# Kernel tuning notes

Measured on AMD Instinct MI355X. Metric: run time of the kernel, lower is better.

The kernel has to match this reference:

```python
import jax, jax.numpy as jnp
import numpy as np

H, D_MODEL, LEN_Q, LEN_K, D_K, D_V = 16, 1024, 512, 2048, 64, 64
B = 4

def setup_inputs() -> dict:
    key = jax.random.key(0)
    ks = jax.random.split(key, 16)
    s = 0.02
    return {
        "Q": jax.random.normal(ks[0], (B, LEN_Q, D_MODEL), jnp.float32),
        "K": jax.random.normal(ks[1], (B, LEN_K, D_MODEL), jnp.float32),
        "V": jax.random.normal(ks[2], (B, LEN_K, D_MODEL), jnp.float32),
        "node_num": LEN_Q,
        "mask": jax.random.randint(ks[3], (B, LEN_K), 0, 2, jnp.int32),
        # params (stored as [in, out] so y = x @ W + b)
        "Wq": jax.random.normal(ks[4], (D_MODEL, H * D_K), jnp.float32) * s,
        "bq": jnp.zeros((H * D_K,), jnp.float32),
        "Wk": jax.random.normal(ks[5], (D_MODEL, H * D_K), jnp.float32) * s,
        "bk": jnp.zeros((H * D_K,), jnp.float32),
        "Wv": jax.random.normal(ks[6], (D_MODEL, H * D_V), jnp.float32) * s,
        "bv": jnp.zeros((H * D_V,), jnp.float32),
        "Wo": jax.random.normal(ks[7], (H * D_V, D_MODEL), jnp.float32) * s,
        "bo": jnp.zeros((D_MODEL,), jnp.float32),
        "gamma": jnp.ones((D_MODEL,), jnp.float32),
        "beta": jnp.zeros((D_MODEL,), jnp.float32),
    }

def _layernorm(x, gamma, beta, eps=1e-5):
    mu = jnp.mean(x, axis=-1, keepdims=True)
    var = jnp.mean((x - mu) ** 2, axis=-1, keepdims=True)
    return (x - mu) * jax.lax.rsqrt(var + eps) * gamma + beta

def reference(Q, K, V, node_num, mask, Wq, bq, Wk, bk, Wv, bv, Wo, bo, gamma, beta):
    b, lq, _ = Q.shape
    lk = K.shape[1]
    q = (Q @ Wq + bq).reshape(b, lq, H, D_K)   # [B, Lq, h, dk]
    k = (K @ Wk + bk).reshape(b, lk, H, D_K)   # [B, Lk, h, dk]
    v = (V @ Wv + bv).reshape(b, lk, H, D_V)   # [B, Lk, h, dv]
    scores = jnp.einsum('bqhd,bkhd->bhqk', q, k) / jnp.sqrt(jnp.float32(D_K))
    scores = jnp.where(mask[:, None, None, :] == 0, -jnp.inf, scores)
    alpha = jax.nn.softmax(scores, axis=-1)    # [B, h, Lq, Lk]
    out = jnp.einsum('bhqk,bkhd->bqhd', alpha, v).reshape(b, lq, H * D_V)
    out = out @ Wo + bo + Q                    # dropout is identity (eval)
    return _layernorm(out, gamma, beta)
```

## Files before the change

### kernel.cpp

```cpp
#include <hip/hip_runtime.h>

typedef __attribute__((ext_vector_type(8))) __bf16 bf16x8;
typedef __attribute__((ext_vector_type(4))) float f32x4;
typedef __attribute__((ext_vector_type(8))) unsigned short u16x8;

__device__ __forceinline__ float bf2f(unsigned short h) {
  union { unsigned int u; float f; } a; a.u = ((unsigned int)h) << 16; return a.f;
}
__device__ __forceinline__ unsigned short f2bf(float f) {
  __bf16 h = (__bf16)f;
  unsigned short u; __builtin_memcpy(&u, &h, 2); return u;
}
__device__ __forceinline__ float fast_exp2(float x) {
#if __has_builtin(__builtin_amdgcn_exp2f)
  return __builtin_amdgcn_exp2f(x);
#else
  return exp2f(x);
#endif
}
__device__ __forceinline__ bf16x8 ld_frag(const unsigned short* p) {
  bf16x8 r; __builtin_memcpy(&r, p, 16); return r;
}
__device__ __forceinline__ void cp16(unsigned short* dst, const unsigned short* src) {
  u16x8 t; __builtin_memcpy(&t, src, 16); __builtin_memcpy(dst, &t, 16);
}

#if __has_builtin(__builtin_amdgcn_global_load_lds)
typedef __attribute__((address_space(3))) unsigned int lds_u32;
typedef const __attribute__((address_space(1))) unsigned int glb_u32;
__device__ __forceinline__ void gload16(const unsigned short* g, unsigned short* l) {
  __builtin_amdgcn_global_load_lds((glb_u32*)g, (lds_u32*)l, 16, 0, 0);
}
#else
__device__ __forceinline__ void gload16(const unsigned short* g, unsigned short* l) {
  cp16(l, g);
}
#endif

__global__ __launch_bounds__(256) void prep_kernel(
    const float* __restrict__ Q, const float* __restrict__ K, const float* __restrict__ V,
    const float* __restrict__ w0, const float* __restrict__ w1,
    const float* __restrict__ w2, const float* __restrict__ w3,
    unsigned short* __restrict__ qb, unsigned short* __restrict__ kb,
    unsigned short* __restrict__ vb, unsigned short* __restrict__ wt)
{
  __shared__ unsigned short tile[64 * 65];
  const int bid = blockIdx.x;
  const int t = threadIdx.x;
  if (bid < 9216) {
    const float* in; unsigned short* out; int i;
    if (bid < 1024)      { in = Q; out = qb; i = bid * 256 + t; }
    else if (bid < 5120) { in = K; out = kb; i = (bid - 1024) * 256 + t; }
    else                 { in = V; out = vb; i = (bid - 5120) * 256 + t; }
    float tf[8]; __builtin_memcpy(tf, &in[(size_t)i * 8], 32);
    unsigned short tu[8];
#pragma unroll
    for (int j = 0; j < 8; j++) tu[j] = f2bf(tf[j]);
    __builtin_memcpy(&out[(size_t)i * 8], tu, 16);
    return;
  }
  const int t4 = bid - 9216;
  const int z = t4 >> 8;
  const float* in = (z == 0) ? w0 : (z == 1) ? w1 : (z == 2) ? w2 : w3;
  unsigned short* o = wt + (size_t)z * 1048576;
  const int dim = 1024;
  const int n0 = (t4 & 15) * 64, k0 = ((t4 >> 4) & 15) * 64;
#pragma unroll
  for (int e = 0; e < 16; e++) {
    int idx = e * 256 + t;
    int i = idx >> 6, j = idx & 63;
    tile[i * 65 + j] = f2bf(in[(size_t)(k0 + i) * dim + n0 + j]);
  }
  __syncthreads();
#pragma unroll
  for (int e = 0; e < 16; e++) {
    int idx = e * 256 + t;
    int i = idx >> 6, j = idx & 63;
    o[(size_t)(n0 + i) * dim + k0 + j] = tile[j * 65 + i];
  }
}

__global__ __launch_bounds__(256, 4) void projqk_kernel(
    const unsigned short* __restrict__ qb,
    const unsigned short* __restrict__ kb,
    const unsigned short* __restrict__ WT4,
    const float* __restrict__ bq, const float* __restrict__ bk,
    unsigned short* __restrict__ qp,
    unsigned short* __restrict__ ktiles)
{
  __shared__ unsigned short pool[12288];
  const int bid = blockIdx.x;
  const int tid  = threadIdx.x;
  const int wave = tid >> 6;
  const int lane = tid & 63;
  const int quad = lane >> 4;
  const int l16  = lane & 15;
  const int K = 1024;
  const f32x4 fz = {0.0f, 0.0f, 0.0f, 0.0f};
  const int srow0 = tid >> 2;
  const int scol  = (tid & 3) * 8;

  if (bid < 512) {
    const int m0 = (bid & 31) * 64;
    const int n0 = (bid >> 5) * 64;
    const int wm = (wave & 1) * 32;
    const int wn = (wave >> 1) * 32;
    f32x4 acc[2][2];
#pragma unroll
    for (int i = 0; i < 2; i++)
#pragma unroll
      for (int j = 0; j < 2; j++) acc[i][j] = fz;

    auto stage = [&](int bf, int k0) {
      unsigned short* Asb = pool + bf * 2048;
      unsigned short* Bsb = pool + 4096 + bf * 2048;
      gload16(&qb[(size_t)(m0 + srow0) * K + k0 + scol], &Asb[srow0 * 32 + scol]);
      gload16(&WT4[(size_t)(n0 + srow0) * K + k0 + scol], &Bsb[srow0 * 32 + scol]);
    };
    const int NT = K >> 5;
    stage(0, 0);
    for (int kt = 0; kt < NT; ++kt) {
      const int cur = kt & 1;
      if (kt + 1 < NT) {
        stage(cur ^ 1, (kt + 1) << 5);
        asm volatile("s_waitcnt vmcnt(2)" ::: "memory");
      } else {
        asm volatile("s_waitcnt vmcnt(0)" ::: "memory");
      }
      __builtin_amdgcn_s_barrier();
      const unsigned short* Asb = pool + cur * 2048;
      const unsigned short* Bsb = pool + 4096 + cur * 2048;
      bf16x8 afr[2], bfr[2];
#pragma unroll
      for (int mt = 0; mt < 2; mt++) afr[mt] = ld_frag(&Asb[(wm + mt * 16 + l16) * 32 + quad * 8]);
#pragma unroll
      for (int nt = 0; nt < 2; nt++) bfr[nt] = ld_frag(&Bsb[(wn + nt * 16 + l16) * 32 + quad * 8]);
#pragma unroll
      for (int mt = 0; mt < 2; mt++)
#pragma unroll
        for (int nt = 0; nt < 2; nt++)
          acc[mt][nt] = __builtin_amdgcn_mfma_f32_16x16x32_bf16(afr[mt], bfr[nt], acc[mt][nt], 0, 0, 0);
      __builtin_amdgcn_s_barrier();
    }
    const float cscale = 0.18033688011112042f;
#pragma unroll
    for (int nt = 0; nt < 2; nt++) {
      int col = n0 + wn + nt * 16 + l16;
      float bv = bq[col];
#pragma unroll
      for (int mt = 0; mt < 2; mt++) {
        int rowb = m0 + wm + mt * 16 + quad * 4;
#pragma unroll
        for (int r = 0; r < 4; r++)
          qp[(size_t)(rowb + r) * 1024 + col] = f2bf((acc[mt][nt][r] + bv) * cscale);
      }
    }
  } else {
    const int tb = bid - 512;
    const int m0 = (tb & 63) * 128;
    const int n0 = (tb >> 6) * 64;
    const int wm = (wave & 1) * 64;
    const int wn = (wave >> 1) * 32;
    const unsigned short* BT = WT4 + 1048576;
    f32x4 acc[4][2];
#pragma unroll
    for (int i = 0; i < 4; i++)
#pragma unroll
      for (int j = 0; j < 2; j++) acc[i][j] = fz;

    const int srow1 = srow0 + 64;
    auto stage = [&](int bf, int k0) {
      unsigned short* Asb = pool + bf * 4096;
      unsigned short* Bsb = pool + 8192 + bf * 2048;
      gload16(&kb[(size_t)(m0 + srow0) * K + k0 + scol], &Asb[srow0 * 32 + scol]);
      gload16(&kb[(size_t)(m0 + srow1) * K + k0 + scol], &Asb[srow1 * 32 + scol]);
      gload16(&BT[(size_t)(n0 + srow0) * K + k0 + scol], &Bsb[srow0 * 32 + scol]);
    };
    const int NT = K >> 5;
    stage(0, 0);
    for (int kt = 0; kt < NT; ++kt) {
      const int cur = kt & 1;
      if (kt + 1 < NT) {
        stage(cur ^ 1, (kt + 1) << 5);
        asm volatile("s_waitcnt vmcnt(3)" ::: "memory");
      } else {
        asm volatile("s_waitcnt vmcnt(0)" ::: "memory");
      }
      __builtin_amdgcn_s_barrier();
      const unsigned short* Asb = pool + cur * 4096;
      const unsigned short* Bsb = pool + 8192 + cur * 2048;
      bf16x8 afr[4], bfr[2];
#pragma unroll
      for (int mt = 0; mt < 4; mt++) afr[mt] = ld_frag(&Asb[(wm + mt * 16 + l16) * 32 + quad * 8]);
#pragma unroll
      for (int nt = 0; nt < 2; nt++) bfr[nt] = ld_frag(&Bsb[(wn + nt * 16 + l16) * 32 + quad * 8]);
#pragma unroll
      for (int mt = 0; mt < 4; mt++)
#pragma unroll
        for (int nt = 0; nt < 2; nt++)
          acc[mt][nt] = __builtin_amdgcn_mfma_f32_16x16x32_bf16(afr[mt], bfr[nt], acc[mt][nt], 0, 0, 0);
      __builtin_amdgcn_s_barrier();
    }
#pragma unroll
    for (int nt = 0; nt < 2; nt++) {
      const int col = n0 + wn + nt * 16 + l16;
      const float bvv = bk[col];
      const int h  = col >> 6;
      const int dk = col & 63;
      const int kc = dk >> 5;
      const int dq = (dk >> 3) & 3;
      const int de = dk & 7;
#pragma unroll
      for (int mt = 0; mt < 4; mt++) {
#pragma unroll
        for (int r = 0; r < 4; r++) {
          const int row = m0 + wm + mt * 16 + quad * 4 + r;
          const int bb = row >> 11, key = row & 2047;
          const size_t tile = ((size_t)((bb * 16 + h) * 32 + (key >> 6))) * 4096;
          const int knt = (key & 63) >> 4;
          const int kl16 = key & 15;
          ktiles[tile + ((size_t)((knt * 2 + kc) * 64 + dq * 16 + kl16)) * 8 + de] =
              f2bf(acc[mt][nt][r] + bvv);
        }
      }
    }
  }
}

__global__ __launch_bounds__(256) void gemm_bt64_kernel(
    const unsigned short* __restrict__ A,
    const unsigned short* __restrict__ BT,
    const float* __restrict__ bias,
    unsigned short* __restrict__ C,
    int M, int N, int K, float cscale)
{
  __shared__ unsigned short As[2][64 * 32];
  __shared__ unsigned short Bs[2][64 * 32];
  const int tid  = threadIdx.x;
  const int wave = tid >> 6;
  const int lane = tid & 63;
  const int quad = lane >> 4;
  const int l16  = lane & 15;
  const int m0 = blockIdx.x * 64;
  const int n0 = blockIdx.y * 64;
  const int wm = (wave & 1) * 32;
  const int wn = (wave >> 1) * 32;

  const f32x4 fz = {0.0f, 0.0f, 0.0f, 0.0f};
  f32x4 acc[2][2];
#pragma unroll
  for (int i = 0; i < 2; i++)
#pragma unroll
    for (int j = 0; j < 2; j++) acc[i][j] = fz;

  const int srow0 = tid >> 2;
  const int scol  = (tid & 3) * 8;

  auto stage = [&](int bf, int k0) {
    gload16(&A[(size_t)(m0 + srow0) * K + k0 + scol], &As[bf][srow0 * 32 + scol]);
    gload16(&BT[(size_t)(n0 + srow0) * K + k0 + scol], &Bs[bf][srow0 * 32 + scol]);
  };

  const int NT = K >> 5;
  stage(0, 0);
  for (int kt = 0; kt < NT; ++kt) {
    const int cur = kt & 1;
    if (kt + 1 < NT) {
      stage(cur ^ 1, (kt + 1) << 5);
      asm volatile("s_waitcnt vmcnt(2)" ::: "memory");
    } else {
      asm volatile("s_waitcnt vmcnt(0)" ::: "memory");
    }
    __builtin_amdgcn_s_barrier();
    bf16x8 afr[2], bfr[2];
#pragma unroll
    for (int mt = 0; mt < 2; mt++) afr[mt] = ld_frag(&As[cur][(wm + mt * 16 + l16) * 32 + quad * 8]);
#pragma unroll
    for (int nt = 0; nt < 2; nt++) bfr[nt] = ld_frag(&Bs[cur][(wn + nt * 16 + l16) * 32 + quad * 8]);
#pragma unroll
    for (int mt = 0; mt < 2; mt++)
#pragma unroll
      for (int nt = 0; nt < 2; nt++)
        acc[mt][nt] = __builtin_amdgcn_mfma_f32_16x16x32_bf16(afr[mt], bfr[nt], acc[mt][nt], 0, 0, 0);
    __builtin_amdgcn_s_barrier();
  }

#pragma unroll
  for (int nt = 0; nt < 2; nt++) {
    int col = n0 + wn + nt * 16 + l16;
    float bv = bias[col];
#pragma unroll
    for (int mt = 0; mt < 2; mt++) {
      int rowb = m0 + wm + mt * 16 + quad * 4;
#pragma unroll
      for (int r = 0; r < 4; r++)
        C[(size_t)(rowb + r) * N + col] = f2bf((acc[mt][nt][r] + bv) * cscale);
    }
  }
}

__global__ __launch_bounds__(256, 4) void gemm_vt_kernel(
    const unsigned short* __restrict__ A,
    const unsigned short* __restrict__ BT,
    const float* __restrict__ bias,
    unsigned short* __restrict__ vt)
{
  __shared__ unsigned short pool[12288];
  const int K = 1024;
  const int tid  = threadIdx.x;
  const int wave = tid >> 6;
  const int lane = tid & 63;
  const int quad = lane >> 4;
  const int l16  = lane & 15;
  const int m0 = blockIdx.x * 128;
  const int n0 = blockIdx.y * 64;
  const int wm = (wave & 1) * 64;
  const int wn = (wave >> 1) * 32;

  const f32x4 fz = {0.0f, 0.0f, 0.0f, 0.0f};
  f32x4 acc[4][2];
#pragma unroll
  for (int i = 0; i < 4; i++)
#pragma unroll
    for (int j = 0; j < 2; j++) acc[i][j] = fz;

  const int srow0 = tid >> 2;
  const int srow1 = srow0 + 64;
  const int scol  = (tid & 3) * 8;

  auto stage = [&](int bf, int k0) {
    unsigned short* Asb = pool + bf * 6144;
    unsigned short* Bsb = Asb + 4096;
    gload16(&A[(size_t)(m0 + srow0) * K + k0 + scol], &Asb[srow0 * 32 + scol]);
    gload16(&A[(size_t)(m0 + srow1) * K + k0 + scol], &Asb[srow1 * 32 + scol]);
    gload16(&BT[(size_t)(n0 + srow0) * K + k0 + scol], &Bsb[srow0 * 32 + scol]);
  };

  const int NT = K >> 5;
  stage(0, 0);
  for (int kt = 0; kt < NT; ++kt) {
    const int cur = kt & 1;
    if (kt + 1 < NT) {
      stage(cur ^ 1, (kt + 1) << 5);
      asm volatile("s_waitcnt vmcnt(3)" ::: "memory");
    } else {
      asm volatile("s_waitcnt vmcnt(0)" ::: "memory");
    }
    __builtin_amdgcn_s_barrier();
    const unsigned short* Asb = pool + cur * 6144;
    const unsigned short* Bsb = Asb + 4096;
    bf16x8 afr[4], bfr[2];
#pragma unroll
    for (int mt = 0; mt < 4; mt++) afr[mt] = ld_frag(&Asb[(wm + mt * 16 + l16) * 32 + quad * 8]);
#pragma unroll
    for (int nt = 0; nt < 2; nt++) bfr[nt] = ld_frag(&Bsb[(wn + nt * 16 + l16) * 32 + quad * 8]);
#pragma unroll
    for (int mt = 0; mt < 4; mt++)
#pragma unroll
      for (int nt = 0; nt < 2; nt++)
        acc[mt][nt] = __builtin_amdgcn_mfma_f32_16x16x32_bf16(afr[mt], bfr[nt], acc[mt][nt], 0, 0, 0);
    __builtin_amdgcn_s_barrier();
  }

  unsigned short* Ts = pool + wave * 2304;
#pragma unroll
  for (int nt = 0; nt < 2; nt++) {
    const float bvv = bias[n0 + wn + nt * 16 + l16];
#pragma unroll
    for (int mt = 0; mt < 4; mt++)
#pragma unroll
      for (int r = 0; r < 4; r++)
        Ts[(nt * 16 + l16) * 72 + mt * 16 + quad * 4 + r] = f2bf(acc[mt][nt][r] + bvv);
  }
  {
    const int R0 = m0 + wm;
    const int b  = R0 >> 11;
    const int ktile = (R0 & 2047) >> 6;
    const int h = n0 >> 6;
    const int dv_local = lane >> 1;
    const int kc = lane & 1;
    const int dv = wn + dv_local;
    const int dvt = dv >> 4, vl16 = dv & 15;
    const size_t vtile = ((size_t)((b * 16 + h) * 32 + ktile)) * 4096;
#pragma unroll
    for (int jb = 0; jb < 4; jb++) {
      const size_t dst = vtile + ((size_t)((dvt * 2 + kc) * 64 + jb * 16 + vl16)) * 8;
      cp16((unsigned short*)&vt[dst], &Ts[dv_local * 72 + kc * 32 + jb * 8]);
    }
  }
}

__global__ __launch_bounds__(512) void attn_kernel(
    const unsigned short* __restrict__ qp,
    const unsigned short* __restrict__ kp,
    const unsigned short* __restrict__ vt,
    const int* __restrict__ mask,
    unsigned short* __restrict__ attn)
{
  __shared__ unsigned short Kb[2][4096];
  __shared__ unsigned short Vb[2][4096];
  __shared__ int Ms[2048];
  __shared__ unsigned short Ps[8][16 * 72];

  const int tid  = threadIdx.x;
  const int wave = tid >> 6;
  const int lane = tid & 63;
  const int quad = lane >> 4;
  const int l16  = lane & 15;
  const int bid  = blockIdx.x;
  const int bh = bid & 63;
  const int qg = bid >> 6;
  const int b = bh >> 4, h = bh & 15;

  bf16x8 aq[2];
  {
    const size_t qbase = ((size_t)(b * 512 + qg * 128 + wave * 16 + l16)) * 1024 + h * 64;
#pragma unroll
    for (int kc = 0; kc < 2; kc++)
      aq[kc] = ld_frag(&qp[qbase + kc * 32 + quad * 8]);
  }
  {
    const unsigned short* mg = (const unsigned short*)(mask + b * 2048);
    unsigned short* ml = (unsigned short*)Ms;
    gload16(mg + tid * 8, ml + tid * 8);
  }
  asm volatile("s_waitcnt vmcnt(0)" ::: "memory");

  const size_t kvbase = (size_t)bh * 131072;
  auto stageKV = [&](int bf, int kt) {
    const unsigned short* ksrc = kp + kvbase + (size_t)kt * 4096;
    const unsigned short* vsrc = vt + kvbase + (size_t)kt * 4096;
    gload16(ksrc + tid * 8, &Kb[bf][tid * 8]);
    gload16(vsrc + tid * 8, &Vb[bf][tid * 8]);
  };

  const f32x4 fz = {0.0f, 0.0f, 0.0f, 0.0f};
  float l_i[4];
  f32x4 O[4];
#pragma unroll
  for (int r = 0; r < 4; r++) { l_i[r] = 0.0f; O[r] = fz; }

  stageKV(0, 0);
  for (int kt = 0; kt < 32; ++kt) {
    const int cur = kt & 1;
    if (kt + 1 < 32) {
      stageKV(cur ^ 1, kt + 1);
      asm volatile("s_waitcnt vmcnt(2)" ::: "memory");
    } else {
      asm volatile("s_waitcnt vmcnt(0)" ::: "memory");
    }
    __builtin_amdgcn_s_barrier();

    int mk[4];
#pragma unroll
    for (int nt = 0; nt < 4; nt++) mk[nt] = Ms[kt * 64 + nt * 16 + l16];

    f32x4 s[4];
#pragma unroll
    for (int nt = 0; nt < 4; nt++) s[nt] = fz;
    __builtin_amdgcn_s_setprio(1);
#pragma unroll
    for (int nt = 0; nt < 4; nt++)
#pragma unroll
      for (int kc = 0; kc < 2; kc++) {
        bf16x8 bk = ld_frag(&Kb[cur][(nt * 2 + kc) * 512 + lane * 8]);
        s[nt] = __builtin_amdgcn_mfma_f32_16x16x32_bf16(aq[kc], bk, s[nt], 0, 0, 0);
      }
    __builtin_amdgcn_s_setprio(0);

#pragma unroll
    for (int nt = 0; nt < 4; nt++) {
      bool ok = (mk[nt] != 0);
#pragma unroll
      for (int r = 0; r < 4; r++) {
        float p = ok ? fast_exp2(s[nt][r]) : 0.0f;
        l_i[r] += p;
        Ps[wave][(quad * 4 + r) * 72 + nt * 16 + l16] = f2bf(p);
      }
    }

    bf16x8 ap[2];
#pragma unroll
    for (int kc = 0; kc < 2; kc++)
      ap[kc] = ld_frag(&Ps[wave][l16 * 72 + kc * 32 + quad * 8]);
    __builtin_amdgcn_s_setprio(1);
#pragma unroll
    for (int dvt = 0; dvt < 4; dvt++)
#pragma unroll
      for (int kc = 0; kc < 2; kc++) {
        bf16x8 bvf = ld_frag(&Vb[cur][(dvt * 2 + kc) * 512 + lane * 8]);
        O[dvt] = __builtin_amdgcn_mfma_f32_16x16x32_bf16(ap[kc], bvf, O[dvt], 0, 0, 0);
      }
    __builtin_amdgcn_s_setprio(0);
    __builtin_amdgcn_s_barrier();
  }

#pragma unroll
  for (int off = 1; off < 16; off <<= 1)
#pragma unroll
    for (int r = 0; r < 4; r++) l_i[r] += __shfl_xor(l_i[r], off);

  const int growb = b * 512 + qg * 128 + wave * 16 + quad * 4;
#pragma unroll
  for (int r = 0; r < 4; r++) {
    const float inv = (l_i[r] > 0.0f) ? (1.0f / l_i[r]) : 0.0f;
#pragma unroll
    for (int dvt = 0; dvt < 4; dvt++)
      attn[(size_t)(growb + r) * 1024 + h * 64 + dvt * 16 + l16] = f2bf(O[dvt][r] * inv);
  }
}

__global__ __launch_bounds__(256) void ln_kernel(
    const unsigned short* __restrict__ x,
    const float* __restrict__ resid,
    const float* __restrict__ gamma,
    const float* __restrict__ beta,
    float* __restrict__ out)
{
  const int row = blockIdx.x;
  const int t = threadIdx.x;
  const int wave = t >> 6, lane = t & 63;
  __shared__ float red[8];
  float v[4];
  float s1 = 0.0f, s2 = 0.0f;
#pragma unroll
  for (int i = 0; i < 4; i++) {
    int e = t + i * 256;
    float val = bf2f(x[(size_t)row * 1024 + e]) + resid[(size_t)row * 1024 + e];
    v[i] = val; s1 += val; s2 += val * val;
  }
#pragma unroll
  for (int off = 1; off < 64; off <<= 1) { s1 += __shfl_xor(s1, off); s2 += __shfl_xor(s2, off); }
  if (lane == 0) { red[wave] = s1; red[4 + wave] = s2; }
  __syncthreads();
  s1 = red[0] + red[1] + red[2] + red[3];
  s2 = red[4] + red[5] + red[6] + red[7];
  float mu  = s1 * (1.0f / 1024.0f);
  float var = s2 * (1.0f / 1024.0f) - mu * mu;
  float rstd = rsqrtf(var + 1e-5f);
#pragma unroll
  for (int i = 0; i < 4; i++) {
    int e = t + i * 256;
    out[(size_t)row * 1024 + e] = (v[i] - mu) * rstd * gamma[e] + beta[e];
  }
}

extern "C" void kernel_launch(void* const* d_in, const int* in_sizes, int n_in,
                              void* d_out, int out_size, void* d_ws, size_t ws_size,
                              hipStream_t stream) {
  (void)out_size; (void)ws_size;
  const float* Q = (const float*)d_in[0];
  const float* K = (const float*)d_in[1];
  const float* V = (const float*)d_in[2];

  int ix = 3;
  if (ix < n_in && in_sizes[ix] == 1) ix++;
  const int* mask  = (const int*)d_in[ix++];
  const float* Wq = (const float*)d_in[ix++]; const float* bq = (const float*)d_in[ix++];
  const float* Wk = (const float*)d_in[ix++]; const float* bk = (const float*)d_in[ix++];
  const float* Wv = (const float*)d_in[ix++]; const float* bv = (const float*)d_in[ix++];
  const float* Wo = (const float*)d_in[ix++]; const float* bo = (const float*)d_in[ix++];
  const float* gm = (const float*)d_in[ix++]; const float* bt = (const float*)d_in[ix++];

  char* ws = (char*)d_ws;
  dim3 blk(256);
  dim3 blk512(512);

  unsigned short* WT4    = (unsigned short*)(ws);
  unsigned short* qp     = (unsigned short*)(ws + (8ull  << 20));
  unsigned short* kb     = (unsigned short*)(ws + (12ull << 20));
  unsigned short* vtiles = kb;
  unsigned short* vb     = (unsigned short*)(ws + (28ull << 20));
  unsigned short* qb     = (unsigned short*)(ws + (44ull << 20));
  unsigned short* at     = qb;
  unsigned short* ktiles = (unsigned short*)(ws + (48ull << 20));

  prep_kernel<<<dim3(10240), blk, 0, stream>>>(Q, K, V, Wq, Wk, Wv, Wo, qb, kb, vb, WT4);
  projqk_kernel<<<dim3(1536), blk, 0, stream>>>(qb, kb, WT4, bq, bk, qp, ktiles);
  gemm_vt_kernel<<<dim3(64, 16), blk, 0, stream>>>(vb, WT4 + 2097152, bv, vtiles);
  attn_kernel<<<dim3(256), blk512, 0, stream>>>(qp, ktiles, vtiles, mask, at);
  gemm_bt64_kernel<<<dim3(32, 16), blk, 0, stream>>>(at, WT4 + 3145728, bo, qp, 2048, 1024, 1024, 1.0f);
  ln_kernel<<<dim3(2048), blk, 0, stream>>>(qp, Q, gm, bt, (float*)d_out);
}
```

Measured before the change: 265.0 us.

## Switch GEMM and attention K/V staging to triple-buffered LDS with one barrier

Every tiled GEMM kernel (Q/K projection, generic bt64 GEMM, V projection) and the attention kernel move from a double buffer to a three-slot LDS ring. Two tiles are prefetched up front, and each iteration issues the load for tile kt+2 after its MFMAs. This lets the trailing per-iteration barrier be dropped, leaving one barrier per step and more load-in-flight distance. The cost is about 50% more shared memory per block, which may limit how many blocks fit per CU, plus a modulo-3 buffer index. The V projection adds an explicit sync before reusing the pool for its transpose.

```diff
diff --git a/kernel.cpp b/kernel.cpp
--- a/kernel.cpp
+++ b/kernel.cpp
@@ -88,7 +88,7 @@
     unsigned short* __restrict__ qp,
     unsigned short* __restrict__ ktiles)
 {
-  __shared__ unsigned short pool[12288];
+  __shared__ unsigned short pool[18432];
   const int bid = blockIdx.x;
   const int tid  = threadIdx.x;
   const int wave = tid >> 6;
@@ -99,6 +99,7 @@
   const f32x4 fz = {0.0f, 0.0f, 0.0f, 0.0f};
   const int srow0 = tid >> 2;
   const int scol  = (tid & 3) * 8;
+  const int NT = K >> 5;
 
   if (bid < 512) {
     const int m0 = (bid & 31) * 64;
@@ -111,25 +112,21 @@
 #pragma unroll
       for (int j = 0; j < 2; j++) acc[i][j] = fz;
 
-    auto stage = [&](int bf, int k0) {
-      unsigned short* Asb = pool + bf * 2048;
-      unsigned short* Bsb = pool + 4096 + bf * 2048;
+    auto stage = [&](int s, int k0) {
+      unsigned short* Asb = pool + s * 2048;
+      unsigned short* Bsb = pool + 6144 + s * 2048;
       gload16(&qb[(size_t)(m0 + srow0) * K + k0 + scol], &Asb[srow0 * 32 + scol]);
       gload16(&WT4[(size_t)(n0 + srow0) * K + k0 + scol], &Bsb[srow0 * 32 + scol]);
     };
-    const int NT = K >> 5;
     stage(0, 0);
+    stage(1, 32);
     for (int kt = 0; kt < NT; ++kt) {
-      const int cur = kt & 1;
-      if (kt + 1 < NT) {
-        stage(cur ^ 1, (kt + 1) << 5);
-        asm volatile("s_waitcnt vmcnt(2)" ::: "memory");
-      } else {
-        asm volatile("s_waitcnt vmcnt(0)" ::: "memory");
-      }
+      if (kt + 1 < NT) asm volatile("s_waitcnt vmcnt(2)" ::: "memory");
+      else             asm volatile("s_waitcnt vmcnt(0)" ::: "memory");
       __builtin_amdgcn_s_barrier();
+      const int cur = kt % 3;
       const unsigned short* Asb = pool + cur * 2048;
-      const unsigned short* Bsb = pool + 4096 + cur * 2048;
+      const unsigned short* Bsb = pool + 6144 + cur * 2048;
       bf16x8 afr[2], bfr[2];
 #pragma unroll
       for (int mt = 0; mt < 2; mt++) afr[mt] = ld_frag(&Asb[(wm + mt * 16 + l16) * 32 + quad * 8]);
@@ -140,19 +137,19 @@
 #pragma unroll
         for (int nt = 0; nt < 2; nt++)
           acc[mt][nt] = __builtin_amdgcn_mfma_f32_16x16x32_bf16(afr[mt], bfr[nt], acc[mt][nt], 0, 0, 0);
-      __builtin_amdgcn_s_barrier();
+      if (kt + 2 < NT) stage((kt + 2) % 3, (kt + 2) << 5);
     }
     const float cscale = 0.18033688011112042f;
 #pragma unroll
     for (int nt = 0; nt < 2; nt++) {
       int col = n0 + wn + nt * 16 + l16;
-      float bv = bq[col];
+      float bsc = bq[col];
 #pragma unroll
       for (int mt = 0; mt < 2; mt++) {
         int rowb = m0 + wm + mt * 16 + quad * 4;
 #pragma unroll
         for (int r = 0; r < 4; r++)
-          qp[(size_t)(rowb + r) * 1024 + col] = f2bf((acc[mt][nt][r] + bv) * cscale);
+          qp[(size_t)(rowb + r) * 1024 + col] = f2bf((acc[mt][nt][r] + bsc) * cscale);
       }
     }
   } else {
@@ -169,26 +166,22 @@
       for (int j = 0; j < 2; j++) acc[i][j] = fz;
 
     const int srow1 = srow0 + 64;
-    auto stage = [&](int bf, int k0) {
-      unsigned short* Asb = pool + bf * 4096;
-      unsigned short* Bsb = pool + 8192 + bf * 2048;
+    auto stage = [&](int s, int k0) {
+      unsigned short* Asb = pool + s * 4096;
+      unsigned short* Bsb = pool + 12288 + s * 2048;
       gload16(&kb[(size_t)(m0 + srow0) * K + k0 + scol], &Asb[srow0 * 32 + scol]);
       gload16(&kb[(size_t)(m0 + srow1) * K + k0 + scol], &Asb[srow1 * 32 + scol]);
       gload16(&BT[(size_t)(n0 + srow0) * K + k0 + scol], &Bsb[srow0 * 32 + scol]);
     };
-    const int NT = K >> 5;
     stage(0, 0);
+    stage(1, 32);
     for (int kt = 0; kt < NT; ++kt) {
-      const int cur = kt & 1;
-      if (kt + 1 < NT) {
-        stage(cur ^ 1, (kt + 1) << 5);
-        asm volatile("s_waitcnt vmcnt(3)" ::: "memory");
-      } else {
-        asm volatile("s_waitcnt vmcnt(0)" ::: "memory");
-      }
+      if (kt + 1 < NT) asm volatile("s_waitcnt vmcnt(3)" ::: "memory");
+      else             asm volatile("s_waitcnt vmcnt(0)" ::: "memory");
       __builtin_amdgcn_s_barrier();
+      const int cur = kt % 3;
       const unsigned short* Asb = pool + cur * 4096;
-      const unsigned short* Bsb = pool + 8192 + cur * 2048;
+      const unsigned short* Bsb = pool + 12288 + cur * 2048;
       bf16x8 afr[4], bfr[2];
 #pragma unroll
       for (int mt = 0; mt < 4; mt++) afr[mt] = ld_frag(&Asb[(wm + mt * 16 + l16) * 32 + quad * 8]);
@@ -199,7 +192,7 @@
 #pragma unroll
         for (int nt = 0; nt < 2; nt++)
           acc[mt][nt] = __builtin_amdgcn_mfma_f32_16x16x32_bf16(afr[mt], bfr[nt], acc[mt][nt], 0, 0, 0);
-      __builtin_amdgcn_s_barrier();
+      if (kt + 2 < NT) stage((kt + 2) % 3, (kt + 2) << 5);
     }
 #pragma unroll
     for (int nt = 0; nt < 2; nt++) {
@@ -234,8 +227,7 @@
     unsigned short* __restrict__ C,
     int M, int N, int K, float cscale)
 {
-  __shared__ unsigned short As[2][64 * 32];
-  __shared__ unsigned short Bs[2][64 * 32];
+  __shared__ unsigned short pool[12288];
   const int tid  = threadIdx.x;
   const int wave = tid >> 6;
   const int lane = tid & 63;
@@ -256,45 +248,46 @@
   const int srow0 = tid >> 2;
   const int scol  = (tid & 3) * 8;
 
-  auto stage = [&](int bf, int k0) {
-    gload16(&A[(size_t)(m0 + srow0) * K + k0 + scol], &As[bf][srow0 * 32 + scol]);
-    gload16(&BT[(size_t)(n0 + srow0) * K + k0 + scol], &Bs[bf][srow0 * 32 + scol]);
+  auto stage = [&](int s, int k0) {
+    unsigned short* Asb = pool + s * 2048;
+    unsigned short* Bsb = pool + 6144 + s * 2048;
+    gload16(&A[(size_t)(m0 + srow0) * K + k0 + scol], &Asb[srow0 * 32 + scol]);
+    gload16(&BT[(size_t)(n0 + srow0) * K + k0 + scol], &Bsb[srow0 * 32 + scol]);
   };
 
   const int NT = K >> 5;
   stage(0, 0);
+  stage(1, 32);
   for (int kt = 0; kt < NT; ++kt) {
-    const int cur = kt & 1;
-    if (kt + 1 < NT) {
-      stage(cur ^ 1, (kt + 1) << 5);
-      asm volatile("s_waitcnt vmcnt(2)" ::: "memory");
-    } else {
-      asm volatile("s_waitcnt vmcnt(0)" ::: "memory");
-    }
+    if (kt + 1 < NT) asm volatile("s_waitcnt vmcnt(2)" ::: "memory");
+    else             asm volatile("s_waitcnt vmcnt(0)" ::: "memory");
     __builtin_amdgcn_s_barrier();
+    const int cur = kt % 3;
+    const unsigned short* Asb = pool + cur * 2048;
+    const unsigned short* Bsb = pool + 6144 + cur * 2048;
     bf16x8 afr[2], bfr[2];
 #pragma unroll
-    for (int mt = 0; mt < 2; mt++) afr[mt] = ld_frag(&As[cur][(wm + mt * 16 + l16) * 32 + quad * 8]);
-#pragma unroll
-    for (int nt = 0; nt < 2; nt++) bfr[nt] = ld_frag(&Bs[cur][(wn + nt * 16 + l16) * 32 + quad * 8]);
+    for (int mt = 0; mt < 2; mt++) afr[mt] = ld_frag(&Asb[(wm + mt * 16 + l16) * 32 + quad * 8]);
+#pragma unroll
+    for (int nt = 0; nt < 2; nt++) bfr[nt] = ld_frag(&Bsb[(wn + nt * 16 + l16) * 32 + quad * 8]);
 #pragma unroll
     for (int mt = 0; mt < 2; mt++)
 #pragma unroll
       for (int nt = 0; nt < 2; nt++)
         acc[mt][nt] = __builtin_amdgcn_mfma_f32_16x16x32_bf16(afr[mt], bfr[nt], acc[mt][nt], 0, 0, 0);
-    __builtin_amdgcn_s_barrier();
+    if (kt + 2 < NT) stage((kt + 2) % 3, (kt + 2) << 5);
   }
 
 #pragma unroll
   for (int nt = 0; nt < 2; nt++) {
     int col = n0 + wn + nt * 16 + l16;
-    float bv = bias[col];
+    float bsc = bias[col];
 #pragma unroll
     for (int mt = 0; mt < 2; mt++) {
       int rowb = m0 + wm + mt * 16 + quad * 4;
 #pragma unroll
       for (int r = 0; r < 4; r++)
-        C[(size_t)(rowb + r) * N + col] = f2bf((acc[mt][nt][r] + bv) * cscale);
+        C[(size_t)(rowb + r) * N + col] = f2bf((acc[mt][nt][r] + bsc) * cscale);
     }
   }
 }
@@ -305,7 +298,7 @@
     const float* __restrict__ bias,
     unsigned short* __restrict__ vt)
 {
-  __shared__ unsigned short pool[12288];
+  __shared__ unsigned short pool[18432];
   const int K = 1024;
   const int tid  = threadIdx.x;
   const int wave = tid >> 6;
@@ -328,9 +321,9 @@
   const int srow1 = srow0 + 64;
   const int scol  = (tid & 3) * 8;
 
-  auto stage = [&](int bf, int k0) {
-    unsigned short* Asb = pool + bf * 6144;
-    unsigned short* Bsb = Asb + 4096;
+  auto stage = [&](int s, int k0) {
+    unsigned short* Asb = pool + s * 4096;
+    unsigned short* Bsb = pool + 12288 + s * 2048;
     gload16(&A[(size_t)(m0 + srow0) * K + k0 + scol], &Asb[srow0 * 32 + scol]);
     gload16(&A[(size_t)(m0 + srow1) * K + k0 + scol], &Asb[srow1 * 32 + scol]);
     gload16(&BT[(size_t)(n0 + srow0) * K + k0 + scol], &Bsb[srow0 * 32 + scol]);
@@ -338,17 +331,14 @@
 
   const int NT = K >> 5;
   stage(0, 0);
+  stage(1, 32);
   for (int kt = 0; kt < NT; ++kt) {
-    const int cur = kt & 1;
-    if (kt + 1 < NT) {
-      stage(cur ^ 1, (kt + 1) << 5);
-      asm volatile("s_waitcnt vmcnt(3)" ::: "memory");
-    } else {
-      asm volatile("s_waitcnt vmcnt(0)" ::: "memory");
-    }
+    if (kt + 1 < NT) asm volatile("s_waitcnt vmcnt(3)" ::: "memory");
+    else             asm volatile("s_waitcnt vmcnt(0)" ::: "memory");
     __builtin_amdgcn_s_barrier();
-    const unsigned short* Asb = pool + cur * 6144;
-    const unsigned short* Bsb = Asb + 4096;
+    const int cur = kt % 3;
+    const unsigned short* Asb = pool + cur * 4096;
+    const unsigned short* Bsb = pool + 12288 + cur * 2048;
     bf16x8 afr[4], bfr[2];
 #pragma unroll
     for (int mt = 0; mt < 4; mt++) afr[mt] = ld_frag(&Asb[(wm + mt * 16 + l16) * 32 + quad * 8]);
@@ -359,8 +349,9 @@
 #pragma unroll
       for (int nt = 0; nt < 2; nt++)
         acc[mt][nt] = __builtin_amdgcn_mfma_f32_16x16x32_bf16(afr[mt], bfr[nt], acc[mt][nt], 0, 0, 0);
-    __builtin_amdgcn_s_barrier();
-  }
+    if (kt + 2 < NT) stage((kt + 2) % 3, (kt + 2) << 5);
+  }
+  __syncthreads();
 
   unsigned short* Ts = pool + wave * 2304;
 #pragma unroll
@@ -397,8 +388,8 @@
     const int* __restrict__ mask,
     unsigned short* __restrict__ attn)
 {
-  __shared__ unsigned short Kb[2][4096];
-  __shared__ unsigned short Vb[2][4096];
+  __shared__ unsigned short Kb[3][4096];
+  __shared__ unsigned short Vb[3][4096];
   __shared__ int Ms[2048];
   __shared__ unsigned short Ps[8][16 * 72];
 
@@ -427,11 +418,11 @@
   asm volatile("s_waitcnt vmcnt(0)" ::: "memory");
 
   const size_t kvbase = (size_t)bh * 131072;
-  auto stageKV = [&](int bf, int kt) {
+  auto stageKV = [&](int s, int kt) {
     const unsigned short* ksrc = kp + kvbase + (size_t)kt * 4096;
     const unsigned short* vsrc = vt + kvbase + (size_t)kt * 4096;
-    gload16(ksrc + tid * 8, &Kb[bf][tid * 8]);
-    gload16(vsrc + tid * 8, &Vb[bf][tid * 8]);
+    gload16(ksrc + tid * 8, &Kb[s][tid * 8]);
+    gload16(vsrc + tid * 8, &Vb[s][tid * 8]);
   };
 
   const f32x4 fz = {0.0f, 0.0f, 0.0f, 0.0f};
@@ -441,15 +432,12 @@
   for (int r = 0; r < 4; r++) { l_i[r] = 0.0f; O[r] = fz; }
 
   stageKV(0, 0);
+  stageKV(1, 1);
   for (int kt = 0; kt < 32; ++kt) {
-    const int cur = kt & 1;
-    if (kt + 1 < 32) {
-      stageKV(cur ^ 1, kt + 1);
-      asm volatile("s_waitcnt vmcnt(2)" ::: "memory");
-    } else {
-      asm volatile("s_waitcnt vmcnt(0)" ::: "memory");
-    }
+    if (kt + 1 < 32) asm volatile("s_waitcnt vmcnt(2)" ::: "memory");
+    else             asm volatile("s_waitcnt vmcnt(0)" ::: "memory");
     __builtin_amdgcn_s_barrier();
+    const int cur = kt % 3;
 
     int mk[4];
 #pragma unroll
@@ -492,7 +480,7 @@
         O[dvt] = __builtin_amdgcn_mfma_f32_16x16x32_bf16(ap[kc], bvf, O[dvt], 0, 0, 0);
       }
     __builtin_amdgcn_s_setprio(0);
-    __builtin_amdgcn_s_barrier();
+    if (kt + 2 < 32) stageKV((kt + 2) % 3, kt + 2);
   }
 
 #pragma unroll
```

Result: faster. 257.2 us (-2.9%).
